# Performance work log

Measured on AMD Instinct MI355X. Metric: run time of the kernel, lower is better.

## Reference

```python
import jax, jax.numpy as jnp
import numpy as np

B = 262144
NODE_ROWS, EDGE_ROWS, D = 19, 36, 4
KEEP = 4


def _make_sparse(key, rows):
    # each sample has exactly KEEP nonzero rows at random (sorted) positions
    k1, k2 = jax.random.split(key)
    perm = jnp.argsort(jax.random.uniform(k1, (B, rows)), axis=1)
    idx = jnp.sort(perm[:, :KEEP], axis=1)                      # (B, KEEP)
    vals = jax.random.normal(k2, (B, KEEP, D), dtype=jnp.float32) + 0.1
    x = jnp.zeros((B, rows, D), dtype=jnp.float32)
    x = x.at[jnp.arange(B)[:, None], idx].set(vals)
    return x.reshape(B, rows * D)


def setup_inputs() -> dict:
    key = jax.random.key(0)
    kn, ke, k1, k2, k3 = jax.random.split(key, 5)
    node = _make_sparse(kn, NODE_ROWS)   # (B, 76)
    edge = _make_sparse(ke, EDGE_ROWS)   # (B, 144)
    # MLP params (torch Linear default-ish init, stored as (in, out))
    def lin(k, fin, fout):
        ka, kb = jax.random.split(k)
        s = 1.0 / np.sqrt(fin)
        W = jax.random.uniform(ka, (fin, fout), jnp.float32, -s, s)
        b = jax.random.uniform(kb, (fout,), jnp.float32, -s, s)
        return W, b
    W1, b1 = lin(k1, 32, 256)
    W2, b2 = lin(k2, 256, 128)
    W3, b3 = lin(k3, 128, 34)
    return {"node": node, "edge": edge, "W1": W1, "b1": b1,
            "W2": W2, "b2": b2, "W3": W3, "b3": b3}


def _compact4(x):
    # x: (B, R, D) -> first 4 nonzero rows per sample, order preserved: (B, 4, D)
    mask = jnp.any(x != 0, axis=-1)                              # (B, R)
    idx = jnp.argsort(~mask, axis=1, stable=True)[:, :KEEP]      # (B, 4)
    return jnp.take_along_axis(x, idx[:, :, None], axis=1)


def reference(node, edge, W1, b1, W2, b2, W3, b3):
    n = _compact4(node.reshape(-1, NODE_ROWS, D))                # (B, 4, 4)
    e = _compact4(edge.reshape(-1, EDGE_ROWS, D))                # (B, 4, 4)
    x = jnp.concatenate([n, e], axis=-2).reshape(-1, 8 * D)      # (B, 32)
    x = jax.nn.relu(x @ W1 + b1)
    x = jax.nn.relu(x @ W2 + b2)
    x = x @ W3 + b3                                              # (B, 34)
    return jax.nn.log_softmax(x, axis=1)
```

## Files before the change

### kernel.cpp

```cpp
#include <hip/hip_runtime.h>
#include <stdint.h>
#include <stddef.h>

typedef __bf16 bf16;
typedef __attribute__((ext_vector_type(8))) __bf16 bf16x8;
typedef __attribute__((ext_vector_type(4))) __bf16 bf16x4;
typedef __attribute__((ext_vector_type(4))) float  f32x4;

#define W1OFF  0
#define W2OFF  (16*1024)
#define W3OFF  (80*1024)
#define BOFF   (92*1024)
#define IMGSZ  (92*1024 + 1728)
#define NCHUNK (IMGSZ/16)
#define PERW   3072
#define LDSSZ  (IMGSZ + 8*PERW)

#define SWZ(s) ((((s)>>1)&3)<<4)

__global__ void prep_kernel(const float* __restrict__ W1, const float* __restrict__ b1,
                            const float* __restrict__ W2, const float* __restrict__ b2,
                            const float* __restrict__ W3, const float* __restrict__ b3,
                            char* __restrict__ img)
{
  int tid = blockIdx.x * 256 + threadIdx.x;
  if (tid < 92 * 64) {
    int fid = tid >> 6, l = tid & 63;
    int m = l & 15, gg = l >> 4;
    const float* W; int stride, n, k0;
    if (fid < 16)      { W = W1; stride = 256; n = fid * 16 + m;            k0 = gg * 8; }
    else if (fid < 80) { int f = fid - 16; W = W2; stride = 128; n = (f >> 3) * 16 + m; k0 = (f & 7) * 32 + gg * 8; }
    else               { int f = fid - 80; W = W3; stride = 34;  n = (f >> 2) * 16 + m; k0 = (f & 3) * 32 + gg * 8; }
    bf16x8 v;
    #pragma unroll
    for (int j = 0; j < 8; ++j) {
      float x = (stride == 34 && n >= 34) ? 0.f : W[(size_t)(k0 + j) * stride + n];
      v[j] = (bf16)x;
    }
    *(bf16x8*)(img + (size_t)tid * 16) = v;
  } else if (tid < 92 * 64 + 432) {
    int i = tid - 92 * 64;
    float v;
    if (i < 256)      v = b1[i];
    else if (i < 384) v = b2[i - 256];
    else              { int j = i - 384; v = (j < 34) ? b3[j] : 0.f; }
    ((float*)(img + BOFF))[i] = v;
  }
}

__global__ __launch_bounds__(512, 2) void mlp_kernel(
    const float* __restrict__ node, const float* __restrict__ edge,
    const char* __restrict__ img, float* __restrict__ out)
{
  __shared__ __align__(16) char sm[LDSSZ];
  const int tid  = threadIdx.x;
  const int lane = tid & 63;
  const int w    = tid >> 6;
  const int blk  = blockIdx.x;

  for (int c = tid; c < NCHUNK; c += 512)
    *(f32x4*)(sm + (size_t)c * 16) = *(const f32x4*)(img + (size_t)c * 16);
  __syncthreads();

  char* const xb0 = sm + IMGSZ + w * PERW;
  char* const xb1 = xb0 + 1024;
  char* const stg = xb0 + 2048;
  const float* const b1p = (const float*)(sm + BOFF);
  const float* const b2p = b1p + 256;
  const float* const b3p = b1p + 384;

  const int g   = lane >> 4;
  const int m16 = lane & 15;
  const int cl  = lane & 3;
  const int sl  = lane >> 2;

  const float4* const np = (const float4*)node;
  const float4* const ep = (const float4*)edge;
  const f32x4 zf = {0.f, 0.f, 0.f, 0.f};

  float4 nf[5], ef[9];

  auto issue_loads = [&](int sbase) {
    const int s = sbase + sl;
    #pragma unroll
    for (int i = 0; i < 5; ++i) {
      const int r = cl + 4 * i;
      nf[i] = (r < 19) ? np[(size_t)s * 19 + r] : make_float4(0.f, 0.f, 0.f, 0.f);
    }
    #pragma unroll
    for (int i = 0; i < 9; ++i)
      ef[i] = ep[(size_t)s * 36 + cl + 4 * i];
  };

  auto compact = [&](char* dst) {
    uint32_t nm = 0; unsigned long long em = 0;
    #pragma unroll
    for (int i = 0; i < 5; ++i) {
      const int r = cl + 4 * i;
      if (r < 19 && (nf[i].x != 0.f || nf[i].y != 0.f || nf[i].z != 0.f || nf[i].w != 0.f))
        nm |= (1u << r);
    }
    #pragma unroll
    for (int i = 0; i < 9; ++i) {
      const int r = cl + 4 * i;
      if (ef[i].x != 0.f || ef[i].y != 0.f || ef[i].z != 0.f || ef[i].w != 0.f)
        em |= (1ull << r);
    }
    nm |= __shfl_xor(nm, 1); nm |= __shfl_xor(nm, 2);
    em |= __shfl_xor(em, 1); em |= __shfl_xor(em, 2);
    bf16x4 zb; zb[0] = (bf16)0.f; zb[1] = (bf16)0.f; zb[2] = (bf16)0.f; zb[3] = (bf16)0.f;
    *(bf16x4*)(dst + sl * 64 + ((8 * cl)      ^ SWZ(sl))) = zb;
    *(bf16x4*)(dst + sl * 64 + ((8 * cl + 32) ^ SWZ(sl))) = zb;
    #pragma unroll
    for (int i = 0; i < 5; ++i) {
      const int r = cl + 4 * i;
      if (r < 19 && ((nm >> r) & 1u)) {
        const int slot = __popc(nm & ((1u << r) - 1u));
        if (slot < 4) {
          bf16x4 pk; pk[0] = (bf16)nf[i].x; pk[1] = (bf16)nf[i].y; pk[2] = (bf16)nf[i].z; pk[3] = (bf16)nf[i].w;
          *(bf16x4*)(dst + sl * 64 + ((8 * slot) ^ SWZ(sl))) = pk;
        }
      }
    }
    #pragma unroll
    for (int i = 0; i < 9; ++i) {
      const int r = cl + 4 * i;
      if ((em >> r) & 1ull) {
        const int slot = __popcll(em & ((1ull << r) - 1ull));
        if (slot < 4) {
          bf16x4 pk; pk[0] = (bf16)ef[i].x; pk[1] = (bf16)ef[i].y; pk[2] = (bf16)ef[i].z; pk[3] = (bf16)ef[i].w;
          *(bf16x4*)(dst + sl * 64 + ((32 + 8 * slot) ^ SWZ(sl))) = pk;
        }
      }
    }
  };

  issue_loads(blk * 1024 + w * 16);
  compact(xb0);

  #pragma unroll 1
  for (int p = 0; p < 8; ++p) {
    char* const xb = (p & 1) ? xb1 : xb0;
    char* const xn = (p & 1) ? xb0 : xb1;
    const int S = blk * 1024 + p * 128 + w * 16;
    const bool pf = (p < 7);

    if (pf) issue_loads(S + 128);
    asm volatile("" ::: "memory");

    bf16x8 xf = *(const bf16x8*)(xb + m16 * 64 + ((16 * g) ^ SWZ(m16)));

    f32x4 acc2[8];
    #pragma unroll
    for (int i = 0; i < 8; ++i) acc2[i] = zf;

    #pragma unroll
    for (int kk = 0; kk < 8; ++kk) {
      #pragma unroll
      for (int t = 0; t < 2; ++t) {
        const int nt1 = kk * 2 + t;
        bf16x8 wf = *(const bf16x8*)(sm + W1OFF + nt1 * 1024 + lane * 16);
        f32x4 d = __builtin_amdgcn_mfma_f32_16x16x32_bf16(wf, xf, zf, 0, 0, 0);
        f32x4 b = *(const f32x4*)(b1p + nt1 * 16 + 4 * g);
        bf16x4 pk;
        #pragma unroll
        for (int r = 0; r < 4; ++r) pk[r] = (bf16)fmaxf(d[r] + b[r], 0.f);
        *(bf16x4*)(stg + m16 * 64 + ((32 * t + 8 * g) ^ SWZ(m16))) = pk;
      }
      bf16x8 sf = *(const bf16x8*)(stg + m16 * 64 + ((16 * g) ^ SWZ(m16)));
      #pragma unroll
      for (int nt2 = 0; nt2 < 8; ++nt2) {
        bf16x8 wf = *(const bf16x8*)(sm + W2OFF + (nt2 * 8 + kk) * 1024 + lane * 16);
        acc2[nt2] = __builtin_amdgcn_mfma_f32_16x16x32_bf16(wf, sf, acc2[nt2], 0, 0, 0);
      }
    }

    f32x4 acc3[3];
    #pragma unroll
    for (int i = 0; i < 3; ++i) acc3[i] = zf;

    #pragma unroll
    for (int k2 = 0; k2 < 4; ++k2) {
      #pragma unroll
      for (int t = 0; t < 2; ++t) {
        const int nt2 = k2 * 2 + t;
        f32x4 b = *(const f32x4*)(b2p + nt2 * 16 + 4 * g);
        bf16x4 pk;
        #pragma unroll
        for (int r = 0; r < 4; ++r) pk[r] = (bf16)fmaxf(acc2[nt2][r] + b[r], 0.f);
        *(bf16x4*)(stg + m16 * 64 + ((32 * t + 8 * g) ^ SWZ(m16))) = pk;
      }
      bf16x8 sf = *(const bf16x8*)(stg + m16 * 64 + ((16 * g) ^ SWZ(m16)));
      #pragma unroll
      for (int nt3 = 0; nt3 < 3; ++nt3) {
        bf16x8 wf = *(const bf16x8*)(sm + W3OFF + (nt3 * 4 + k2) * 1024 + lane * 16);
        acc3[nt3] = __builtin_amdgcn_mfma_f32_16x16x32_bf16(wf, sf, acc3[nt3], 0, 0, 0);
      }
    }

    float z[12];
    #pragma unroll
    for (int nt3 = 0; nt3 < 3; ++nt3) {
      f32x4 b = *(const f32x4*)(b3p + nt3 * 16 + 4 * g);
      #pragma unroll
      for (int r = 0; r < 4; ++r) {
        const int f = nt3 * 16 + 4 * g + r;
        z[nt3 * 4 + r] = (f < 34) ? (acc3[nt3][r] + b[r]) : -1e30f;
      }
    }
    float mx = z[0];
    #pragma unroll
    for (int i = 1; i < 12; ++i) mx = fmaxf(mx, z[i]);
    mx = fmaxf(mx, __shfl_xor(mx, 16));
    mx = fmaxf(mx, __shfl_xor(mx, 32));
    float sum = 0.f;
    #pragma unroll
    for (int i = 0; i < 12; ++i) sum += __expf(z[i] - mx);
    sum += __shfl_xor(sum, 16);
    sum += __shfl_xor(sum, 32);
    const float lse = mx + __logf(sum);

    float* orow = out + (size_t)(S + m16) * 34;
    *(float2*)(orow +  0 + 4 * g) = make_float2(z[0] - lse, z[1] - lse);
    *(float2*)(orow +  2 + 4 * g) = make_float2(z[2] - lse, z[3] - lse);
    *(float2*)(orow + 16 + 4 * g) = make_float2(z[4] - lse, z[5] - lse);
    *(float2*)(orow + 18 + 4 * g) = make_float2(z[6] - lse, z[7] - lse);
    if (g == 0)
      *(float2*)(orow + 32) = make_float2(z[8] - lse, z[9] - lse);

    if (pf) compact(xn);
  }
}

extern "C" void kernel_launch(void* const* d_in, const int* in_sizes, int n_in,
                              void* d_out, int out_size, void* d_ws, size_t ws_size,
                              hipStream_t stream)
{
  const float* node = (const float*)d_in[0];
  const float* edge = (const float*)d_in[1];
  const float* W1   = (const float*)d_in[2];
  const float* b1   = (const float*)d_in[3];
  const float* W2   = (const float*)d_in[4];
  const float* b2   = (const float*)d_in[5];
  const float* W3   = (const float*)d_in[6];
  const float* b3   = (const float*)d_in[7];
  char* img = (char*)d_ws;

  prep_kernel<<<25, 256, 0, stream>>>(W1, b1, W2, b2, W3, b3, img);
  mlp_kernel<<<256, 512, 0, stream>>>(node, edge, img, (float*)d_out);
}
```

Before: 62.10 us.

## Process two 16-sample tiles per wave, dropping software prefetch pipeline

Each wave now handles 32 samples per iteration as two independent 16-sample tiles (A and B) that share every weight fragment read from LDS. This halves LDS weight traffic per sample and gives two independent MFMA chains to interleave. The cross-iteration prefetch of the next tile's node/edge inputs is removed, so global load latency is no longer hidden behind compute except through other waves. Register use roughly doubles for the accumulators, and per-wave LDS scratch grows to fit a second staging buffer.

```diff
diff --git a/kernel.cpp b/kernel.cpp
--- a/kernel.cpp
+++ b/kernel.cpp
@@ -13,7 +13,7 @@
 #define BOFF   (92*1024)
 #define IMGSZ  (92*1024 + 1728)
 #define NCHUNK (IMGSZ/16)
-#define PERW   3072
+#define PERW   4096
 #define LDSSZ  (IMGSZ + 8*PERW)
 
 #define SWZ(s) ((((s)>>1)&3)<<4)
@@ -62,9 +62,10 @@
     *(f32x4*)(sm + (size_t)c * 16) = *(const f32x4*)(img + (size_t)c * 16);
   __syncthreads();
 
-  char* const xb0 = sm + IMGSZ + w * PERW;
-  char* const xb1 = xb0 + 1024;
-  char* const stg = xb0 + 2048;
+  char* const xwA  = sm + IMGSZ + w * PERW;
+  char* const xwB  = xwA + 1024;
+  char* const stgA = xwA + 2048;
+  char* const stgB = xwA + 3072;
   const float* const b1p = (const float*)(sm + BOFF);
   const float* const b2p = b1p + 256;
   const float* const b3p = b1p + 384;
@@ -78,9 +79,7 @@
   const float4* const ep = (const float4*)edge;
   const f32x4 zf = {0.f, 0.f, 0.f, 0.f};
 
-  float4 nf[5], ef[9];
-
-  auto issue_loads = [&](int sbase) {
+  auto issue_loads = [&](int sbase, float4* nf, float4* ef) {
     const int s = sbase + sl;
     #pragma unroll
     for (int i = 0; i < 5; ++i) {
@@ -92,7 +91,7 @@
       ef[i] = ep[(size_t)s * 36 + cl + 4 * i];
   };
 
-  auto compact = [&](char* dst) {
+  auto compact = [&](char* dst, const float4* nf, const float4* ef) {
     uint32_t nm = 0; unsigned long long em = 0;
     #pragma unroll
     for (int i = 0; i < 5; ++i) {
@@ -135,24 +134,24 @@
     }
   };
 
-  issue_loads(blk * 1024 + w * 16);
-  compact(xb0);
-
   #pragma unroll 1
-  for (int p = 0; p < 8; ++p) {
-    char* const xb = (p & 1) ? xb1 : xb0;
-    char* const xn = (p & 1) ? xb0 : xb1;
-    const int S = blk * 1024 + p * 128 + w * 16;
-    const bool pf = (p < 7);
-
-    if (pf) issue_loads(S + 128);
-    asm volatile("" ::: "memory");
-
-    bf16x8 xf = *(const bf16x8*)(xb + m16 * 64 + ((16 * g) ^ SWZ(m16)));
-
-    f32x4 acc2[8];
-    #pragma unroll
-    for (int i = 0; i < 8; ++i) acc2[i] = zf;
+  for (int p = 0; p < 4; ++p) {
+    const int S = blk * 1024 + p * 256 + w * 32;
+
+    {
+      float4 nfA[5], efA[9], nfB[5], efB[9];
+      issue_loads(S,      nfA, efA);
+      issue_loads(S + 16, nfB, efB);
+      compact(xwA, nfA, efA);
+      compact(xwB, nfB, efB);
+    }
+
+    bf16x8 xfA = *(const bf16x8*)(xwA + m16 * 64 + ((16 * g) ^ SWZ(m16)));
+    bf16x8 xfB = *(const bf16x8*)(xwB + m16 * 64 + ((16 * g) ^ SWZ(m16)));
+
+    f32x4 accA[8], accB[8];
+    #pragma unroll
+    for (int i = 0; i < 8; ++i) { accA[i] = zf; accB[i] = zf; }
 
     #pragma unroll
     for (int kk = 0; kk < 8; ++kk) {
@@ -160,24 +159,31 @@
       for (int t = 0; t < 2; ++t) {
         const int nt1 = kk * 2 + t;
         bf16x8 wf = *(const bf16x8*)(sm + W1OFF + nt1 * 1024 + lane * 16);
-        f32x4 d = __builtin_amdgcn_mfma_f32_16x16x32_bf16(wf, xf, zf, 0, 0, 0);
+        f32x4 dA = __builtin_amdgcn_mfma_f32_16x16x32_bf16(wf, xfA, zf, 0, 0, 0);
+        f32x4 dB = __builtin_amdgcn_mfma_f32_16x16x32_bf16(wf, xfB, zf, 0, 0, 0);
         f32x4 b = *(const f32x4*)(b1p + nt1 * 16 + 4 * g);
-        bf16x4 pk;
+        bf16x4 pkA, pkB;
         #pragma unroll
-        for (int r = 0; r < 4; ++r) pk[r] = (bf16)fmaxf(d[r] + b[r], 0.f);
-        *(bf16x4*)(stg + m16 * 64 + ((32 * t + 8 * g) ^ SWZ(m16))) = pk;
-      }
-      bf16x8 sf = *(const bf16x8*)(stg + m16 * 64 + ((16 * g) ^ SWZ(m16)));
+        for (int r = 0; r < 4; ++r) {
+          pkA[r] = (bf16)fmaxf(dA[r] + b[r], 0.f);
+          pkB[r] = (bf16)fmaxf(dB[r] + b[r], 0.f);
+        }
+        *(bf16x4*)(stgA + m16 * 64 + ((32 * t + 8 * g) ^ SWZ(m16))) = pkA;
+        *(bf16x4*)(stgB + m16 * 64 + ((32 * t + 8 * g) ^ SWZ(m16))) = pkB;
+      }
+      bf16x8 sfA = *(const bf16x8*)(stgA + m16 * 64 + ((16 * g) ^ SWZ(m16)));
+      bf16x8 sfB = *(const bf16x8*)(stgB + m16 * 64 + ((16 * g) ^ SWZ(m16)));
       #pragma unroll
       for (int nt2 = 0; nt2 < 8; ++nt2) {
         bf16x8 wf = *(const bf16x8*)(sm + W2OFF + (nt2 * 8 + kk) * 1024 + lane * 16);
-        acc2[nt2] = __builtin_amdgcn_mfma_f32_16x16x32_bf16(wf, sf, acc2[nt2], 0, 0, 0);
-      }
-    }
-
-    f32x4 acc3[3];
-    #pragma unroll
-    for (int i = 0; i < 3; ++i) acc3[i] = zf;
+        accA[nt2] = __builtin_amdgcn_mfma_f32_16x16x32_bf16(wf, sfA, accA[nt2], 0, 0, 0);
+        accB[nt2] = __builtin_amdgcn_mfma_f32_16x16x32_bf16(wf, sfB, accB[nt2], 0, 0, 0);
+      }
+    }
+
+    f32x4 acc3A[3], acc3B[3];
+    #pragma unroll
+    for (int i = 0; i < 3; ++i) { acc3A[i] = zf; acc3B[i] = zf; }
 
     #pragma unroll
     for (int k2 = 0; k2 < 4; ++k2) {
@@ -185,50 +191,58 @@
       for (int t = 0; t < 2; ++t) {
         const int nt2 = k2 * 2 + t;
         f32x4 b = *(const f32x4*)(b2p + nt2 * 16 + 4 * g);
-        bf16x4 pk;
+        bf16x4 pkA, pkB;
         #pragma unroll
-        for (int r = 0; r < 4; ++r) pk[r] = (bf16)fmaxf(acc2[nt2][r] + b[r], 0.f);
-        *(bf16x4*)(stg + m16 * 64 + ((32 * t + 8 * g) ^ SWZ(m16))) = pk;
-      }
-      bf16x8 sf = *(const bf16x8*)(stg + m16 * 64 + ((16 * g) ^ SWZ(m16)));
+        for (int r = 0; r < 4; ++r) {
+          pkA[r] = (bf16)fmaxf(accA[nt2][r] + b[r], 0.f);
+          pkB[r] = (bf16)fmaxf(accB[nt2][r] + b[r], 0.f);
+        }
+        *(bf16x4*)(stgA + m16 * 64 + ((32 * t + 8 * g) ^ SWZ(m16))) = pkA;
+        *(bf16x4*)(stgB + m16 * 64 + ((32 * t + 8 * g) ^ SWZ(m16))) = pkB;
+      }
+      bf16x8 sfA = *(const bf16x8*)(stgA + m16 * 64 + ((16 * g) ^ SWZ(m16)));
+      bf16x8 sfB = *(const bf16x8*)(stgB + m16 * 64 + ((16 * g) ^ SWZ(m16)));
       #pragma unroll
       for (int nt3 = 0; nt3 < 3; ++nt3) {
         bf16x8 wf = *(const bf16x8*)(sm + W3OFF + (nt3 * 4 + k2) * 1024 + lane * 16);
-        acc3[nt3] = __builtin_amdgcn_mfma_f32_16x16x32_bf16(wf, sf, acc3[nt3], 0, 0, 0);
-      }
-    }
-
-    float z[12];
-    #pragma unroll
-    for (int nt3 = 0; nt3 < 3; ++nt3) {
-      f32x4 b = *(const f32x4*)(b3p + nt3 * 16 + 4 * g);
-      #pragma unroll
-      for (int r = 0; r < 4; ++r) {
-        const int f = nt3 * 16 + 4 * g + r;
-        z[nt3 * 4 + r] = (f < 34) ? (acc3[nt3][r] + b[r]) : -1e30f;
-      }
-    }
-    float mx = z[0];
-    #pragma unroll
-    for (int i = 1; i < 12; ++i) mx = fmaxf(mx, z[i]);
-    mx = fmaxf(mx, __shfl_xor(mx, 16));
-    mx = fmaxf(mx, __shfl_xor(mx, 32));
-    float sum = 0.f;
-    #pragma unroll
-    for (int i = 0; i < 12; ++i) sum += __expf(z[i] - mx);
-    sum += __shfl_xor(sum, 16);
-    sum += __shfl_xor(sum, 32);
-    const float lse = mx + __logf(sum);
-
-    float* orow = out + (size_t)(S + m16) * 34;
-    *(float2*)(orow +  0 + 4 * g) = make_float2(z[0] - lse, z[1] - lse);
-    *(float2*)(orow +  2 + 4 * g) = make_float2(z[2] - lse, z[3] - lse);
-    *(float2*)(orow + 16 + 4 * g) = make_float2(z[4] - lse, z[5] - lse);
-    *(float2*)(orow + 18 + 4 * g) = make_float2(z[6] - lse, z[7] - lse);
-    if (g == 0)
-      *(float2*)(orow + 32) = make_float2(z[8] - lse, z[9] - lse);
-
-    if (pf) compact(xn);
+        acc3A[nt3] = __builtin_amdgcn_mfma_f32_16x16x32_bf16(wf, sfA, acc3A[nt3], 0, 0, 0);
+        acc3B[nt3] = __builtin_amdgcn_mfma_f32_16x16x32_bf16(wf, sfB, acc3B[nt3], 0, 0, 0);
+      }
+    }
+
+    #pragma unroll
+    for (int tb = 0; tb < 2; ++tb) {
+      const f32x4* a3 = tb ? acc3B : acc3A;
+      float z[12];
+      #pragma unroll
+      for (int nt3 = 0; nt3 < 3; ++nt3) {
+        f32x4 b = *(const f32x4*)(b3p + nt3 * 16 + 4 * g);
+        #pragma unroll
+        for (int r = 0; r < 4; ++r) {
+          const int f = nt3 * 16 + 4 * g + r;
+          z[nt3 * 4 + r] = (f < 34) ? (a3[nt3][r] + b[r]) : -1e30f;
+        }
+      }
+      float mx = z[0];
+      #pragma unroll
+      for (int i = 1; i < 12; ++i) mx = fmaxf(mx, z[i]);
+      mx = fmaxf(mx, __shfl_xor(mx, 16));
+      mx = fmaxf(mx, __shfl_xor(mx, 32));
+      float sum = 0.f;
+      #pragma unroll
+      for (int i = 0; i < 12; ++i) sum += __expf(z[i] - mx);
+      sum += __shfl_xor(sum, 16);
+      sum += __shfl_xor(sum, 32);
+      const float lse = mx + __logf(sum);
+
+      float* orow = out + (size_t)(S + tb * 16 + m16) * 34;
+      *(float2*)(orow +  0 + 4 * g) = make_float2(z[0] - lse, z[1] - lse);
+      *(float2*)(orow +  2 + 4 * g) = make_float2(z[2] - lse, z[3] - lse);
+      *(float2*)(orow + 16 + 4 * g) = make_float2(z[4] - lse, z[5] - lse);
+      *(float2*)(orow + 18 + 4 * g) = make_float2(z[6] - lse, z[7] - lse);
+      if (g == 0)
+        *(float2*)(orow + 32) = make_float2(z[8] - lse, z[9] - lse);
+    }
   }
 }
 
```

Result: slower. 64.47 us (+3.8%).

## Feed MFMA outputs directly as 16x16x16 operands, removing LDS staging of activations

Applied to the files above, without the earlier changes.

Layers 2 and 3 now use 16x16x16 bf16 MFMAs whose B-operand layout matches the accumulator layout of the previous MFMA. Each lane can therefore pack its ReLU'd outputs straight into the next matmul without a store/reload through an LDS staging buffer. The weight image is re-laid out in the prep kernel for the K=16 fragments, and the per-wave LDS buffer shrinks. Waves also start on staggered sample groups, which spreads out global memory access. The cost is twice as many MFMA instructions, each with half the K depth.

```diff
diff --git a/kernel.cpp b/kernel.cpp
--- a/kernel.cpp
+++ b/kernel.cpp
@@ -5,6 +5,7 @@
 typedef __bf16 bf16;
 typedef __attribute__((ext_vector_type(8))) __bf16 bf16x8;
 typedef __attribute__((ext_vector_type(4))) __bf16 bf16x4;
+typedef __attribute__((ext_vector_type(4))) short short4_t;
 typedef __attribute__((ext_vector_type(4))) float  f32x4;
 
 #define W1OFF  0
@@ -13,10 +14,27 @@
 #define BOFF   (92*1024)
 #define IMGSZ  (92*1024 + 1728)
 #define NCHUNK (IMGSZ/16)
-#define PERW   3072
+#define PERW   2048
 #define LDSSZ  (IMGSZ + 8*PERW)
 
 #define SWZ(s) ((((s)>>1)&3)<<4)
+
+#if !defined(__HIP_DEVICE_COMPILE__)
+static __device__ __forceinline__ f32x4 mfma16(bf16x4 a, bf16x4 b, f32x4 c) {
+  (void)a; (void)b; return c;
+}
+#elif __has_builtin(__builtin_amdgcn_mfma_f32_16x16x16_bf16)
+static __device__ __forceinline__ f32x4 mfma16(bf16x4 a, bf16x4 b, f32x4 c) {
+  return __builtin_amdgcn_mfma_f32_16x16x16_bf16(a, b, c, 0, 0, 0);
+}
+#elif __has_builtin(__builtin_amdgcn_mfma_f32_16x16x16bf16_1k)
+static __device__ __forceinline__ f32x4 mfma16(bf16x4 a, bf16x4 b, f32x4 c) {
+  return __builtin_amdgcn_mfma_f32_16x16x16bf16_1k(
+      __builtin_bit_cast(short4_t, a), __builtin_bit_cast(short4_t, b), c, 0, 0, 0);
+}
+#else
+#error "no 16x16x16 bf16 mfma builtin on this toolchain (device pass)"
+#endif
 
 __global__ void prep_kernel(const float* __restrict__ W1, const float* __restrict__ b1,
                             const float* __restrict__ W2, const float* __restrict__ b2,
@@ -24,22 +42,32 @@
                             char* __restrict__ img)
 {
   int tid = blockIdx.x * 256 + threadIdx.x;
-  if (tid < 92 * 64) {
+  if (tid < 1024) {
     int fid = tid >> 6, l = tid & 63;
-    int m = l & 15, gg = l >> 4;
-    const float* W; int stride, n, k0;
-    if (fid < 16)      { W = W1; stride = 256; n = fid * 16 + m;            k0 = gg * 8; }
-    else if (fid < 80) { int f = fid - 16; W = W2; stride = 128; n = (f >> 3) * 16 + m; k0 = (f & 7) * 32 + gg * 8; }
-    else               { int f = fid - 80; W = W3; stride = 34;  n = (f >> 2) * 16 + m; k0 = (f & 3) * 32 + gg * 8; }
+    int n = fid * 16 + (l & 15), k0 = 8 * (l >> 4);
     bf16x8 v;
     #pragma unroll
-    for (int j = 0; j < 8; ++j) {
-      float x = (stride == 34 && n >= 34) ? 0.f : W[(size_t)(k0 + j) * stride + n];
-      v[j] = (bf16)x;
-    }
+    for (int j = 0; j < 8; ++j) v[j] = (bf16)W1[(size_t)(k0 + j) * 256 + n];
     *(bf16x8*)(img + (size_t)tid * 16) = v;
-  } else if (tid < 92 * 64 + 432) {
-    int i = tid - 92 * 64;
+  } else if (tid < 1024 + 8192) {
+    int e = tid - 1024, frag = e >> 6, l = e & 63;
+    int nt2 = frag >> 4, c = frag & 15;
+    int n = nt2 * 16 + (l & 15), k0 = c * 16 + 4 * (l >> 4);
+    bf16x4 v;
+    #pragma unroll
+    for (int j = 0; j < 4; ++j) v[j] = (bf16)W2[(size_t)(k0 + j) * 128 + n];
+    *(bf16x4*)(img + W2OFF + (size_t)e * 8) = v;
+  } else if (tid < 1024 + 8192 + 1536) {
+    int e = tid - 9216, frag = e >> 6, l = e & 63;
+    int nt3 = frag >> 3, c2 = frag & 7;
+    int n = nt3 * 16 + (l & 15), k0 = c2 * 16 + 4 * (l >> 4);
+    bf16x4 v;
+    #pragma unroll
+    for (int j = 0; j < 4; ++j)
+      v[j] = (n < 34) ? (bf16)W3[(size_t)(k0 + j) * 34 + n] : (bf16)0.f;
+    *(bf16x4*)(img + W3OFF + (size_t)e * 8) = v;
+  } else if (tid < 1024 + 8192 + 1536 + 432) {
+    int i = tid - 10752;
     float v;
     if (i < 256)      v = b1[i];
     else if (i < 384) v = b2[i - 256];
@@ -64,7 +92,6 @@
 
   char* const xb0 = sm + IMGSZ + w * PERW;
   char* const xb1 = xb0 + 1024;
-  char* const stg = xb0 + 2048;
   const float* const b1p = (const float*)(sm + BOFF);
   const float* const b2p = b1p + 256;
   const float* const b3p = b1p + 384;
@@ -79,6 +106,8 @@
   const f32x4 zf = {0.f, 0.f, 0.f, 0.f};
 
   float4 nf[5], ef[9];
+
+  auto sample_of = [&](int p) { return blk * 1024 + (((p + w) & 7) * 128) + w * 16; };
 
   auto issue_loads = [&](int sbase) {
     const int s = sbase + sl;
@@ -135,17 +164,17 @@
     }
   };
 
-  issue_loads(blk * 1024 + w * 16);
+  issue_loads(sample_of(0));
   compact(xb0);
 
   #pragma unroll 1
   for (int p = 0; p < 8; ++p) {
     char* const xb = (p & 1) ? xb1 : xb0;
     char* const xn = (p & 1) ? xb0 : xb1;
-    const int S = blk * 1024 + p * 128 + w * 16;
+    const int S = sample_of(p);
     const bool pf = (p < 7);
 
-    if (pf) issue_loads(S + 128);
+    if (pf) issue_loads(sample_of(p + 1));
     asm volatile("" ::: "memory");
 
     bf16x8 xf = *(const bf16x8*)(xb + m16 * 64 + ((16 * g) ^ SWZ(m16)));
@@ -154,24 +183,18 @@
     #pragma unroll
     for (int i = 0; i < 8; ++i) acc2[i] = zf;
 
-    #pragma unroll
-    for (int kk = 0; kk < 8; ++kk) {
-      #pragma unroll
-      for (int t = 0; t < 2; ++t) {
-        const int nt1 = kk * 2 + t;
-        bf16x8 wf = *(const bf16x8*)(sm + W1OFF + nt1 * 1024 + lane * 16);
-        f32x4 d = __builtin_amdgcn_mfma_f32_16x16x32_bf16(wf, xf, zf, 0, 0, 0);
-        f32x4 b = *(const f32x4*)(b1p + nt1 * 16 + 4 * g);
-        bf16x4 pk;
-        #pragma unroll
-        for (int r = 0; r < 4; ++r) pk[r] = (bf16)fmaxf(d[r] + b[r], 0.f);
-        *(bf16x4*)(stg + m16 * 64 + ((32 * t + 8 * g) ^ SWZ(m16))) = pk;
-      }
-      bf16x8 sf = *(const bf16x8*)(stg + m16 * 64 + ((16 * g) ^ SWZ(m16)));
+    #pragma unroll 2
+    for (int c = 0; c < 16; ++c) {
+      bf16x8 wf1 = *(const bf16x8*)(sm + W1OFF + c * 1024 + lane * 16);
+      f32x4 d = __builtin_amdgcn_mfma_f32_16x16x32_bf16(wf1, xf, zf, 0, 0, 0);
+      f32x4 b = *(const f32x4*)(b1p + c * 16 + 4 * g);
+      bf16x4 h1p;
+      #pragma unroll
+      for (int r = 0; r < 4; ++r) h1p[r] = (bf16)fmaxf(d[r] + b[r], 0.f);
       #pragma unroll
       for (int nt2 = 0; nt2 < 8; ++nt2) {
-        bf16x8 wf = *(const bf16x8*)(sm + W2OFF + (nt2 * 8 + kk) * 1024 + lane * 16);
-        acc2[nt2] = __builtin_amdgcn_mfma_f32_16x16x32_bf16(wf, sf, acc2[nt2], 0, 0, 0);
+        bf16x4 w2f = *(const bf16x4*)(sm + W2OFF + (size_t)((nt2 * 16 + c) * 512) + lane * 8);
+        acc2[nt2] = mfma16(w2f, h1p, acc2[nt2]);
       }
     }
 
@@ -180,21 +203,15 @@
     for (int i = 0; i < 3; ++i) acc3[i] = zf;
 
     #pragma unroll
-    for (int k2 = 0; k2 < 4; ++k2) {
-      #pragma unroll
-      for (int t = 0; t < 2; ++t) {
-        const int nt2 = k2 * 2 + t;
-        f32x4 b = *(const f32x4*)(b2p + nt2 * 16 + 4 * g);
-        bf16x4 pk;
-        #pragma unroll
-        for (int r = 0; r < 4; ++r) pk[r] = (bf16)fmaxf(acc2[nt2][r] + b[r], 0.f);
-        *(bf16x4*)(stg + m16 * 64 + ((32 * t + 8 * g) ^ SWZ(m16))) = pk;
-      }
-      bf16x8 sf = *(const bf16x8*)(stg + m16 * 64 + ((16 * g) ^ SWZ(m16)));
+    for (int c2 = 0; c2 < 8; ++c2) {
+      f32x4 b = *(const f32x4*)(b2p + c2 * 16 + 4 * g);
+      bf16x4 h2p;
+      #pragma unroll
+      for (int r = 0; r < 4; ++r) h2p[r] = (bf16)fmaxf(acc2[c2][r] + b[r], 0.f);
       #pragma unroll
       for (int nt3 = 0; nt3 < 3; ++nt3) {
-        bf16x8 wf = *(const bf16x8*)(sm + W3OFF + (nt3 * 4 + k2) * 1024 + lane * 16);
-        acc3[nt3] = __builtin_amdgcn_mfma_f32_16x16x32_bf16(wf, sf, acc3[nt3], 0, 0, 0);
+        bf16x4 w3f = *(const bf16x4*)(sm + W3OFF + (size_t)((nt3 * 8 + c2) * 512) + lane * 8);
+        acc3[nt3] = mfma16(w3f, h2p, acc3[nt3]);
       }
     }
 
@@ -246,6 +263,6 @@
   const float* b3   = (const float*)d_in[7];
   char* img = (char*)d_ws;
 
-  prep_kernel<<<25, 256, 0, stream>>>(W1, b1, W2, b2, W3, b3, img);
+  prep_kernel<<<44, 256, 0, stream>>>(W1, b1, W2, b2, W3, b3, img);
   mlp_kernel<<<256, 512, 0, stream>>>(node, edge, img, (float*)d_out);
 }
```

Result: slower. 69.77 us (+12.4%).

## Switch MLP to 32x32x16 MFMA tiles with bias-initialized accumulators

Applied to the files above, without the earlier changes.

Replaces the 16x16x32 bf16 MFMA tiling with 32x32x16 MFMAs, so each wave processes 32 samples per iteration, and repacks the weight and bias images to match the new fragment layout. Biases are preloaded into the accumulators instead of being added after each layer. The double-buffered prefetch of the next batch's node/edge inputs is removed: loads and compaction now run synchronously at the start of each iteration. This trades memory latency hiding for fewer MFMA issues and less bias arithmetic, and raises register pressure from the 16-wide accumulators.

```diff
diff --git a/kernel.cpp b/kernel.cpp
--- a/kernel.cpp
+++ b/kernel.cpp
@@ -6,17 +6,22 @@
 typedef __attribute__((ext_vector_type(8))) __bf16 bf16x8;
 typedef __attribute__((ext_vector_type(4))) __bf16 bf16x4;
 typedef __attribute__((ext_vector_type(4))) float  f32x4;
+typedef __attribute__((ext_vector_type(16))) float f32x16;
 
 #define W1OFF  0
 #define W2OFF  (16*1024)
 #define W3OFF  (80*1024)
-#define BOFF   (92*1024)
-#define IMGSZ  (92*1024 + 1728)
+#define BIOFF  (96*1024)
+#define BI2OFF (BIOFF + 1024)
+#define BI3OFF (BIOFF + 1536)
+#define IMGSZ  (96*1024 + 1792)
 #define NCHUNK (IMGSZ/16)
-#define PERW   3072
+#define PERW   4096
 #define LDSSZ  (IMGSZ + 8*PERW)
 
 #define SWZ(s) ((((s)>>1)&3)<<4)
+
+#define MFMA32(a,b,c) __builtin_amdgcn_mfma_f32_32x32x16_bf16((a),(b),(c),0,0,0)
 
 __global__ void prep_kernel(const float* __restrict__ W1, const float* __restrict__ b1,
                             const float* __restrict__ W2, const float* __restrict__ b2,
@@ -24,27 +29,46 @@
                             char* __restrict__ img)
 {
   int tid = blockIdx.x * 256 + threadIdx.x;
-  if (tid < 92 * 64) {
-    int fid = tid >> 6, l = tid & 63;
-    int m = l & 15, gg = l >> 4;
-    const float* W; int stride, n, k0;
-    if (fid < 16)      { W = W1; stride = 256; n = fid * 16 + m;            k0 = gg * 8; }
-    else if (fid < 80) { int f = fid - 16; W = W2; stride = 128; n = (f >> 3) * 16 + m; k0 = (f & 7) * 32 + gg * 8; }
-    else               { int f = fid - 80; W = W3; stride = 34;  n = (f >> 2) * 16 + m; k0 = (f & 3) * 32 + gg * 8; }
+  if (tid < 1024) {
+    int frag = tid >> 6, l = tid & 63;
+    int c = frag >> 1, t = frag & 1, hi = l >> 5;
+    int n = c * 32 + (l & 31), k0 = t * 16 + 8 * hi;
     bf16x8 v;
     #pragma unroll
-    for (int j = 0; j < 8; ++j) {
-      float x = (stride == 34 && n >= 34) ? 0.f : W[(size_t)(k0 + j) * stride + n];
-      v[j] = (bf16)x;
-    }
+    for (int j = 0; j < 8; ++j) v[j] = (bf16)W1[(size_t)(k0 + j) * 256 + n];
     *(bf16x8*)(img + (size_t)tid * 16) = v;
-  } else if (tid < 92 * 64 + 432) {
-    int i = tid - 92 * 64;
+  } else if (tid < 5120) {
+    int e = tid - 1024, frag = e >> 6, l = e & 63;
+    int nt2 = frag >> 4, c = (frag >> 1) & 7, t = frag & 1, hi = l >> 5;
+    int n = nt2 * 32 + (l & 31), k0 = c * 32 + t * 16 + 8 * hi;
+    bf16x8 v;
+    #pragma unroll
+    for (int j = 0; j < 8; ++j) v[j] = (bf16)W2[(size_t)(k0 + j) * 128 + n];
+    *(bf16x8*)(img + W2OFF + (size_t)e * 16) = v;
+  } else if (tid < 6144) {
+    int e = tid - 5120, frag = e >> 6, l = e & 63;
+    int nt3 = frag >> 3, c2 = (frag >> 1) & 3, t = frag & 1, hi = l >> 5;
+    int n = nt3 * 32 + (l & 31), k0 = c2 * 32 + t * 16 + 8 * hi;
+    bf16x8 v;
+    #pragma unroll
+    for (int j = 0; j < 8; ++j)
+      v[j] = (n < 34) ? (bf16)W3[(size_t)(k0 + j) * 34 + n] : (bf16)0.f;
+    *(bf16x8*)(img + W3OFF + (size_t)e * 16) = v;
+  } else if (tid < 6144 + 448) {
+    int e = tid - 6144;
+    int le, chunk, idx; const float* bsrc; char* dst; int nb;
+    if (e < 256)      { le = e;       bsrc = b1; dst = img + BIOFF;  nb = 34; chunk = le >> 5; }
+    else if (e < 384) { le = e - 256; bsrc = b2; dst = img + BI2OFF; nb = 1000; chunk = le >> 5; }
+    else              { le = e - 384; bsrc = b3; dst = img + BI3OFF; nb = 34; chunk = le >> 5; }
+    idx = le & 31;
+    int hi = idx >> 4, reg = idx & 15;
+    int f = chunk * 32 + (reg & 3) + 8 * (reg >> 2) + 4 * hi;
     float v;
-    if (i < 256)      v = b1[i];
-    else if (i < 384) v = b2[i - 256];
-    else              { int j = i - 384; v = (j < 34) ? b3[j] : 0.f; }
-    ((float*)(img + BOFF))[i] = v;
+    if (e < 256)      v = b1[f];
+    else if (e < 384) v = b2[f];
+    else              v = (f < 34) ? b3[f] : 0.f;
+    (void)bsrc; (void)nb;
+    ((float*)dst)[le] = v;
   }
 }
 
@@ -62,21 +86,17 @@
     *(f32x4*)(sm + (size_t)c * 16) = *(const f32x4*)(img + (size_t)c * 16);
   __syncthreads();
 
-  char* const xb0 = sm + IMGSZ + w * PERW;
-  char* const xb1 = xb0 + 1024;
-  char* const stg = xb0 + 2048;
-  const float* const b1p = (const float*)(sm + BOFF);
-  const float* const b2p = b1p + 256;
-  const float* const b3p = b1p + 384;
-
-  const int g   = lane >> 4;
-  const int m16 = lane & 15;
+  char* const xw  = sm + IMGSZ + w * PERW;
+  char* const stg = xw + 2048;
+
+  const int col = lane & 31;
+  const int hi  = lane >> 5;
+  const int swz = (col >> 1) & 3;
   const int cl  = lane & 3;
   const int sl  = lane >> 2;
 
   const float4* const np = (const float4*)node;
   const float4* const ep = (const float4*)edge;
-  const f32x4 zf = {0.f, 0.f, 0.f, 0.f};
 
   float4 nf[5], ef[9];
 
@@ -135,100 +155,99 @@
     }
   };
 
-  issue_loads(blk * 1024 + w * 16);
-  compact(xb0);
+  auto ldbias = [&](const char* p) -> f32x16 {
+    const f32x4* q4 = (const f32x4*)(p + hi * 64);
+    f32x4 q0 = q4[0], q1 = q4[1], q2 = q4[2], q3 = q4[3];
+    f32x16 r;
+    #pragma unroll
+    for (int i = 0; i < 4; ++i) { r[i] = q0[i]; r[4+i] = q1[i]; r[8+i] = q2[i]; r[12+i] = q3[i]; }
+    return r;
+  };
 
   #pragma unroll 1
-  for (int p = 0; p < 8; ++p) {
-    char* const xb = (p & 1) ? xb1 : xb0;
-    char* const xn = (p & 1) ? xb0 : xb1;
-    const int S = blk * 1024 + p * 128 + w * 16;
-    const bool pf = (p < 7);
-
-    if (pf) issue_loads(S + 128);
-    asm volatile("" ::: "memory");
-
-    bf16x8 xf = *(const bf16x8*)(xb + m16 * 64 + ((16 * g) ^ SWZ(m16)));
-
-    f32x4 acc2[8];
-    #pragma unroll
-    for (int i = 0; i < 8; ++i) acc2[i] = zf;
-
-    #pragma unroll
-    for (int kk = 0; kk < 8; ++kk) {
-      #pragma unroll
-      for (int t = 0; t < 2; ++t) {
-        const int nt1 = kk * 2 + t;
-        bf16x8 wf = *(const bf16x8*)(sm + W1OFF + nt1 * 1024 + lane * 16);
-        f32x4 d = __builtin_amdgcn_mfma_f32_16x16x32_bf16(wf, xf, zf, 0, 0, 0);
-        f32x4 b = *(const f32x4*)(b1p + nt1 * 16 + 4 * g);
+  for (int p = 0; p < 4; ++p) {
+    const int S = blk * 1024 + p * 256 + w * 32;
+
+    issue_loads(S);       compact(xw);
+    issue_loads(S + 16);  compact(xw + 1024);
+
+    bf16x8 xf0 = *(const bf16x8*)(xw + col * 64 + ((hi * 16)      ^ SWZ(col)));
+    bf16x8 xf1 = *(const bf16x8*)(xw + col * 64 + ((32 + hi * 16) ^ SWZ(col)));
+
+    f32x16 acc2[4];
+    #pragma unroll
+    for (int nt2 = 0; nt2 < 4; ++nt2) acc2[nt2] = ldbias(sm + BI2OFF + nt2 * 128);
+
+    #pragma unroll 1
+    for (int c = 0; c < 8; ++c) {
+      __builtin_amdgcn_sched_barrier(0);
+      f32x16 d = ldbias(sm + BIOFF + c * 128);
+      bf16x8 w10 = *(const bf16x8*)(sm + W1OFF + (c * 2 + 0) * 1024 + lane * 16);
+      bf16x8 w11 = *(const bf16x8*)(sm + W1OFF + (c * 2 + 1) * 1024 + lane * 16);
+      d = MFMA32(w10, xf0, d);
+      d = MFMA32(w11, xf1, d);
+      #pragma unroll
+      for (int q = 0; q < 4; ++q) {
         bf16x4 pk;
         #pragma unroll
-        for (int r = 0; r < 4; ++r) pk[r] = (bf16)fmaxf(d[r] + b[r], 0.f);
-        *(bf16x4*)(stg + m16 * 64 + ((32 * t + 8 * g) ^ SWZ(m16))) = pk;
-      }
-      bf16x8 sf = *(const bf16x8*)(stg + m16 * 64 + ((16 * g) ^ SWZ(m16)));
-      #pragma unroll
-      for (int nt2 = 0; nt2 < 8; ++nt2) {
-        bf16x8 wf = *(const bf16x8*)(sm + W2OFF + (nt2 * 8 + kk) * 1024 + lane * 16);
-        acc2[nt2] = __builtin_amdgcn_mfma_f32_16x16x32_bf16(wf, sf, acc2[nt2], 0, 0, 0);
-      }
-    }
-
-    f32x4 acc3[3];
-    #pragma unroll
-    for (int i = 0; i < 3; ++i) acc3[i] = zf;
-
-    #pragma unroll
-    for (int k2 = 0; k2 < 4; ++k2) {
-      #pragma unroll
-      for (int t = 0; t < 2; ++t) {
-        const int nt2 = k2 * 2 + t;
-        f32x4 b = *(const f32x4*)(b2p + nt2 * 16 + 4 * g);
+        for (int i = 0; i < 4; ++i) pk[i] = (bf16)fmaxf(d[4 * q + i], 0.f);
+        *(bf16x4*)(stg + col * 64 + (((q ^ swz) << 4) + hi * 8)) = pk;
+      }
+      bf16x8 sf0 = *(const bf16x8*)(stg + col * 64 + (((0 + hi) ^ swz) << 4));
+      bf16x8 sf1 = *(const bf16x8*)(stg + col * 64 + (((2 + hi) ^ swz) << 4));
+      #pragma unroll
+      for (int nt2 = 0; nt2 < 4; ++nt2) {
+        bf16x8 a0 = *(const bf16x8*)(sm + W2OFF + ((nt2 * 8 + c) * 2 + 0) * 1024 + lane * 16);
+        bf16x8 a1 = *(const bf16x8*)(sm + W2OFF + ((nt2 * 8 + c) * 2 + 1) * 1024 + lane * 16);
+        acc2[nt2] = MFMA32(a0, sf0, acc2[nt2]);
+        acc2[nt2] = MFMA32(a1, sf1, acc2[nt2]);
+      }
+    }
+
+    f32x16 acc3[2];
+    acc3[0] = ldbias(sm + BI3OFF + 0);
+    acc3[1] = ldbias(sm + BI3OFF + 128);
+
+    #pragma unroll
+    for (int c2 = 0; c2 < 4; ++c2) {
+      #pragma unroll
+      for (int q = 0; q < 4; ++q) {
         bf16x4 pk;
         #pragma unroll
-        for (int r = 0; r < 4; ++r) pk[r] = (bf16)fmaxf(acc2[nt2][r] + b[r], 0.f);
-        *(bf16x4*)(stg + m16 * 64 + ((32 * t + 8 * g) ^ SWZ(m16))) = pk;
-      }
-      bf16x8 sf = *(const bf16x8*)(stg + m16 * 64 + ((16 * g) ^ SWZ(m16)));
-      #pragma unroll
-      for (int nt3 = 0; nt3 < 3; ++nt3) {
-        bf16x8 wf = *(const bf16x8*)(sm + W3OFF + (nt3 * 4 + k2) * 1024 + lane * 16);
-        acc3[nt3] = __builtin_amdgcn_mfma_f32_16x16x32_bf16(wf, sf, acc3[nt3], 0, 0, 0);
-      }
-    }
-
-    float z[12];
-    #pragma unroll
-    for (int nt3 = 0; nt3 < 3; ++nt3) {
-      f32x4 b = *(const f32x4*)(b3p + nt3 * 16 + 4 * g);
-      #pragma unroll
-      for (int r = 0; r < 4; ++r) {
-        const int f = nt3 * 16 + 4 * g + r;
-        z[nt3 * 4 + r] = (f < 34) ? (acc3[nt3][r] + b[r]) : -1e30f;
-      }
-    }
-    float mx = z[0];
-    #pragma unroll
-    for (int i = 1; i < 12; ++i) mx = fmaxf(mx, z[i]);
-    mx = fmaxf(mx, __shfl_xor(mx, 16));
+        for (int i = 0; i < 4; ++i) pk[i] = (bf16)fmaxf(acc2[c2][4 * q + i], 0.f);
+        *(bf16x4*)(stg + col * 64 + (((q ^ swz) << 4) + hi * 8)) = pk;
+      }
+      bf16x8 sf0 = *(const bf16x8*)(stg + col * 64 + (((0 + hi) ^ swz) << 4));
+      bf16x8 sf1 = *(const bf16x8*)(stg + col * 64 + (((2 + hi) ^ swz) << 4));
+      #pragma unroll
+      for (int nt3 = 0; nt3 < 2; ++nt3) {
+        bf16x8 a0 = *(const bf16x8*)(sm + W3OFF + ((nt3 * 4 + c2) * 2 + 0) * 1024 + lane * 16);
+        bf16x8 a1 = *(const bf16x8*)(sm + W3OFF + ((nt3 * 4 + c2) * 2 + 1) * 1024 + lane * 16);
+        acc3[nt3] = MFMA32(a0, sf0, acc3[nt3]);
+        acc3[nt3] = MFMA32(a1, sf1, acc3[nt3]);
+      }
+    }
+
+    float mx = acc3[0][0];
+    #pragma unroll
+    for (int i = 1; i < 16; ++i) mx = fmaxf(mx, acc3[0][i]);
+    if (hi == 0) { mx = fmaxf(mx, acc3[1][0]); mx = fmaxf(mx, acc3[1][1]); }
     mx = fmaxf(mx, __shfl_xor(mx, 32));
     float sum = 0.f;
     #pragma unroll
-    for (int i = 0; i < 12; ++i) sum += __expf(z[i] - mx);
-    sum += __shfl_xor(sum, 16);
+    for (int i = 0; i < 16; ++i) sum += __expf(acc3[0][i] - mx);
+    if (hi == 0) sum += __expf(acc3[1][0] - mx) + __expf(acc3[1][1] - mx);
     sum += __shfl_xor(sum, 32);
     const float lse = mx + __logf(sum);
 
-    float* orow = out + (size_t)(S + m16) * 34;
-    *(float2*)(orow +  0 + 4 * g) = make_float2(z[0] - lse, z[1] - lse);
-    *(float2*)(orow +  2 + 4 * g) = make_float2(z[2] - lse, z[3] - lse);
-    *(float2*)(orow + 16 + 4 * g) = make_float2(z[4] - lse, z[5] - lse);
-    *(float2*)(orow + 18 + 4 * g) = make_float2(z[6] - lse, z[7] - lse);
-    if (g == 0)
-      *(float2*)(orow + 32) = make_float2(z[8] - lse, z[9] - lse);
-
-    if (pf) compact(xn);
+    float* orow = out + (size_t)(S + col) * 34;
+    #pragma unroll
+    for (int q = 0; q < 4; ++q) {
+      *(float2*)(orow + 8 * q + 4 * hi)     = make_float2(acc3[0][4 * q]     - lse, acc3[0][4 * q + 1] - lse);
+      *(float2*)(orow + 8 * q + 4 * hi + 2) = make_float2(acc3[0][4 * q + 2] - lse, acc3[0][4 * q + 3] - lse);
+    }
+    if (hi == 0)
+      *(float2*)(orow + 32) = make_float2(acc3[1][0] - lse, acc3[1][1] - lse);
   }
 }
 
@@ -246,6 +265,6 @@
   const float* b3   = (const float*)d_in[7];
   char* img = (char*)d_ws;
 
-  prep_kernel<<<25, 256, 0, stream>>>(W1, b1, W2, b2, W3, b3, img);
+  prep_kernel<<<26, 256, 0, stream>>>(W1, b1, W2, b2, W3, b3, img);
   mlp_kernel<<<256, 512, 0, stream>>>(node, edge, img, (float*)d_out);
 }
```

Result: slower. 66.23 us (+6.7%).
